# Optimization experiments

Measured on AMD Instinct MI355X. Metric: run time of the kernel, lower is better.

## Reference

```python
import jax, jax.numpy as jnp
import numpy as np

N = 50000        # nodes
E = 400000       # edges (avg degree 8)
T = 4            # edge types
D_IN = 64        # input feature dim
D_OUT = 128      # GGNN hidden / output dim
B = 64           # graphs in batch
STEPS = 8        # GRU propagation steps


def setup_inputs() -> dict:
    key = jax.random.key(0)
    ks = jax.random.split(key, 10)
    s = 1.0 / np.sqrt(D_OUT)
    features = jax.random.normal(ks[0], (N, D_IN), jnp.float32)
    src = jax.random.randint(ks[1], (E,), 0, N, jnp.int32)
    dst = jax.random.randint(ks[2], (E,), 0, N, jnp.int32)
    etype = jax.random.randint(ks[3], (E,), 0, T, jnp.int32)
    node2graph = jnp.sort(jax.random.randint(ks[4], (N,), 0, B, jnp.int32))
    # per-edge-type message Linear(out, out)
    W_msg = jax.random.normal(ks[5], (T, D_OUT, D_OUT), jnp.float32) * s
    b_msg = jnp.zeros((T, D_OUT), jnp.float32)
    # GRUCell(out, out): gate order (r, z, n) as in torch
    w_ih = jax.random.normal(ks[6], (D_OUT, 3 * D_OUT), jnp.float32) * s
    b_ih = jnp.zeros((3 * D_OUT,), jnp.float32)
    w_hh = jax.random.normal(ks[7], (D_OUT, 3 * D_OUT), jnp.float32) * s
    b_hh = jnp.zeros((3 * D_OUT,), jnp.float32)
    # classifier Linear(out, 2)
    W_cls = jax.random.normal(ks[8], (D_OUT, 2), jnp.float32) * s
    b_cls = jnp.zeros((2,), jnp.float32)
    return {"features": features, "src": src, "dst": dst, "etype": etype,
            "node2graph": node2graph, "W_msg": W_msg, "b_msg": b_msg,
            "w_ih": w_ih, "b_ih": b_ih, "w_hh": w_hh, "b_hh": b_hh,
            "W_cls": W_cls, "b_cls": b_cls}


def reference(features, src, dst, etype, node2graph, W_msg, b_msg,
              w_ih, b_ih, w_hh, b_hh, W_cls, b_cls):
    n = features.shape[0]
    # zero-pad input features to D_OUT (as in GGNN.forward)
    h1 = jnp.concatenate(
        [features, jnp.zeros((n, D_OUT - D_IN), features.dtype)], axis=-1)

    def step(h, _):
        # transform every node by every etype weight: [N, T, D]
        t = jnp.einsum('nd,tde->nte', h, W_msg) + b_msg
        msgs = t[src, etype]                       # [E, D] gather per edge
        a = jax.ops.segment_sum(msgs, dst, num_segments=n)  # scatter-sum
        # torch GRUCell(a, h), gates ordered (r, z, n)
        gi = a @ w_ih + b_ih
        gh = h @ w_hh + b_hh
        i_r, i_z, i_n = jnp.split(gi, 3, axis=-1)
        h_r, h_z, h_n = jnp.split(gh, 3, axis=-1)
        r = jax.nn.sigmoid(i_r + h_r)
        z = jax.nn.sigmoid(i_z + h_z)
        ng = jnp.tanh(i_n + r * h_n)
        return (1.0 - z) * ng + z * h, None

    h, _ = jax.lax.scan(step, h1, None, length=STEPS)
    hres = h + h1                                   # residual as in forward
    # read_out == 'sum': per-graph segment sum (dgl.sum_nodes)
    feats_g = jax.ops.segment_sum(hres, node2graph, num_segments=B)  # [B, D]
    return feats_g @ W_cls + b_cls                  # [B, 2]
```

## Files before the change

kernel.cpp:

```cpp
#include <hip/hip_runtime.h>
#include <hip/hip_bf16.h>
#include <math.h>

#define NN 50000
#define EE 400000
#define TT 4
#define DIN 64
#define DD 128
#define BB 64
#define STEPS 8
#define KAGG 544
#define NGATES 512
#define NBIN (4 * NN)
#define NBLK ((NBIN + 255) / 256)
#define MT64 ((NN + 63) / 64)
#define W2F_N (21 * 12288)

typedef __attribute__((ext_vector_type(8))) short bf16x8;
typedef __attribute__((ext_vector_type(4))) float f32x4;
typedef __attribute__((address_space(3))) void lds_void;
typedef __attribute__((address_space(1))) void glob_void;

__device__ inline float bf2f(__hip_bfloat16 x) { return __bfloat162float(x); }

__device__ inline float s2f(short s) {
    unsigned int u = ((unsigned int)(unsigned short)s) << 16;
    float f;
    __builtin_memcpy(&f, &u, 4);
    return f;
}

__global__ void k_init_h(const float* __restrict__ feat, float* __restrict__ h1,
                         __hip_bfloat16* __restrict__ hb) {
    int idx = blockIdx.x * blockDim.x + threadIdx.x;
    if (idx >= NN * DD) return;
    int v = idx >> 7, d = idx & 127;
    float val = (d < DIN) ? feat[v * DIN + d] : 0.0f;
    h1[idx] = val;
    hb[idx] = __float2bfloat16(val);
}

__global__ void k_zero_i32(int* __restrict__ p, int n) {
    int idx = blockIdx.x * blockDim.x + threadIdx.x;
    if (idx < n) p[idx] = 0;
}
__global__ void k_zero_f32(float* __restrict__ p, int n) {
    int idx = blockIdx.x * blockDim.x + threadIdx.x;
    if (idx < n) p[idx] = 0.0f;
}

__global__ void k_hist(const int* __restrict__ dst, const int* __restrict__ etype,
                       int* __restrict__ deg2) {
    int e = blockIdx.x * blockDim.x + threadIdx.x;
    if (e < EE) atomicAdd(&deg2[dst[e] * 4 + etype[e]], 1);
}

__global__ __launch_bounds__(256) void k_scan_bsum(const int* __restrict__ deg2,
                                                   int* __restrict__ bsum) {
    __shared__ int red[256];
    int tid = threadIdx.x;
    int i = blockIdx.x * 256 + tid;
    int v = (i < NBIN) ? deg2[i] : 0;
    red[tid] = v;
    __syncthreads();
#pragma unroll
    for (int s = 128; s > 0; s >>= 1) {
        if (tid < s) red[tid] += red[tid + s];
        __syncthreads();
    }
    if (tid == 0) bsum[blockIdx.x] = red[0];
}

__global__ __launch_bounds__(1024) void k_scan_boff(const int* __restrict__ bsum,
                                                    int* __restrict__ boff) {
    __shared__ int s[1024];
    int tid = threadIdx.x;
    int v = (tid < NBLK) ? bsum[tid] : 0;
    s[tid] = v;
    __syncthreads();
    for (int d = 1; d < 1024; d <<= 1) {
        int t = (tid >= d) ? s[tid - d] : 0;
        __syncthreads();
        s[tid] += t;
        __syncthreads();
    }
    if (tid < NBLK) boff[tid] = s[tid] - v;
}

__global__ __launch_bounds__(256) void k_scan_final(const int* __restrict__ deg2,
                                                    const int* __restrict__ boff,
                                                    int* __restrict__ off2,
                                                    int* __restrict__ cursor) {
    __shared__ int s[256];
    int tid = threadIdx.x;
    int i = blockIdx.x * 256 + tid;
    int v = (i < NBIN) ? deg2[i] : 0;
    s[tid] = v;
    __syncthreads();
#pragma unroll
    for (int d = 1; d < 256; d <<= 1) {
        int t = (tid >= d) ? s[tid - d] : 0;
        __syncthreads();
        s[tid] += t;
        __syncthreads();
    }
    int excl = boff[blockIdx.x] + s[tid] - v;
    if (i < NBIN) {
        off2[i] = excl;
        cursor[i] = excl;
        if (i == NBIN - 1) off2[NBIN] = excl + v;
    }
}

__global__ void k_fill(const int* __restrict__ dst, const int* __restrict__ src,
                       const int* __restrict__ etype, int* __restrict__ cursor,
                       int* __restrict__ csr_src) {
    int e = blockIdx.x * blockDim.x + threadIdx.x;
    if (e < EE) {
        int pos = atomicAdd(&cursor[dst[e] * 4 + etype[e]], 1);
        csr_src[pos] = src[e];
    }
}

__global__ void k_counts(const int* __restrict__ off2, __hip_bfloat16* __restrict__ g) {
    int idx = blockIdx.x * blockDim.x + threadIdx.x;
    if (idx >= NN * 16) return;
    int v = idx >> 4, j = idx & 15;
    float x = 0.0f, y = 0.0f;
    if (j < 2) {
        int t0 = 2 * j;
        x = (float)(off2[4 * v + t0 + 1] - off2[4 * v + t0]);
        y = (float)(off2[4 * v + t0 + 2] - off2[4 * v + t0 + 1]);
    }
    __hip_bfloat162 o;
    o.x = __float2bfloat16(x);
    o.y = __float2bfloat16(y);
    ((__hip_bfloat162*)(g + (size_t)v * KAGG))[256 + j] = o;
}

__global__ void k_prep_w2f(const float* __restrict__ Wm, const float* __restrict__ bm,
                           const float* __restrict__ wih, const float* __restrict__ whh,
                           const float* __restrict__ bih, const float* __restrict__ bhh,
                           __hip_bfloat16* __restrict__ W2f, float* __restrict__ bias512) {
    int idx = blockIdx.x * blockDim.x + threadIdx.x;
    if (idx < W2F_N) {
        int kc = idx / 12288;
        int r1 = idx % 12288;
        int gb = r1 >> 12;
        int r2 = r1 & 4095;
        int w = r2 >> 9;
        int r3 = r2 & 511;
        int l = r3 >> 3;
        int j = r3 & 7;
        int npart = w * 16 + (l & 15);
        int kin = ((l >> 4) << 3) + j;
        float v = 0.0f;
        if (kc < 17) {
            int k = kc * 32 + kin;
            int n = gb * 128 + npart;
            if (k < 512) {
                int t = k >> 7, kd = k & 127;
                const float* wr = Wm + (t << 14) + (kd << 7);
                float s = 0.0f;
#pragma unroll 4
                for (int e = 0; e < 128; ++e) s += wr[e] * wih[e * 384 + n];
                v = s;
            } else if (k < 516) {
                const float* br = bm + ((k - 512) << 7);
                float s = 0.0f;
#pragma unroll 4
                for (int e = 0; e < 128; ++e) s += br[e] * wih[e * 384 + n];
                v = s;
            }
        } else {
            int kh = (kc - 17) * 32 + kin;
            int nlog = (gb < 2) ? gb * 128 + npart : 384 + npart;
            int col = (nlog < 256) ? nlog : nlog - 128;
            v = whh[kh * 384 + col];
        }
        W2f[idx] = __float2bfloat16(v);
        return;
    }
    int b = idx - W2F_N;
    if (b < NGATES) {
        float v;
        if (b < 256) v = bih[b] + bhh[b];
        else if (b < 384) v = bih[b];
        else v = bhh[b - 128];
        bias512[b] = v;
    }
}

__global__ __launch_bounds__(256) void k_agg(const __hip_bfloat16* __restrict__ hb,
                                             const int* __restrict__ off2,
                                             const int* __restrict__ csr_src,
                                             __hip_bfloat16* __restrict__ g) {
    const int node = (blockIdx.x * blockDim.x + threadIdx.x) >> 6;
    const int lane = threadIdx.x & 63;
    if (node >= NN) return;
    const int t = lane >> 4;
    const int sub = lane & 15;
    const int p0 = off2[4 * node + t];
    const int p1 = off2[4 * node + t + 1];
    float a[8];
#pragma unroll
    for (int j = 0; j < 8; ++j) a[j] = 0.0f;
    int p = p0;
    for (; p + 1 < p1; p += 2) {
        int s0 = csr_src[p];
        int s1 = csr_src[p + 1];
        bf16x8 v0 = *(const bf16x8*)(hb + (size_t)s0 * DD + sub * 8);
        bf16x8 v1 = *(const bf16x8*)(hb + (size_t)s1 * DD + sub * 8);
#pragma unroll
        for (int j = 0; j < 8; ++j) a[j] += s2f(v0[j]) + s2f(v1[j]);
    }
    if (p < p1) {
        int s0 = csr_src[p];
        bf16x8 v0 = *(const bf16x8*)(hb + (size_t)s0 * DD + sub * 8);
#pragma unroll
        for (int j = 0; j < 8; ++j) a[j] += s2f(v0[j]);
    }
    bf16x8 o;
#pragma unroll
    for (int j = 0; j < 8; ++j) {
        __hip_bfloat16 b = __float2bfloat16(a[j]);
        o[j] = *(short*)&b;
    }
    *(bf16x8*)(g + (size_t)node * KAGG + t * 128 + sub * 8) = o;
}

__global__ __launch_bounds__(512, 4) void k_step(const __hip_bfloat16* __restrict__ g,
                                                 const __hip_bfloat16* __restrict__ W2f,
                                                 const float* __restrict__ bias512,
                                                 const __hip_bfloat16* __restrict__ hbi,
                                                 __hip_bfloat16* __restrict__ hbo) {
    __shared__ __align__(16) short As[2][64 * 32];
    __shared__ __align__(16) short Ht[64 * 132];
    const int tid = threadIdx.x;
    const int lane = tid & 63;
    const int wave = tid >> 6;
    const int row0 = blockIdx.x * 64;
    const int quad = lane >> 4;
    const int m16 = lane & 15;
    const int koff = ((quad ^ ((m16 ^ (m16 >> 2)) & 3)) << 3);

    const int arow = tid >> 2;
    const int apart = (tid & 3) ^ ((arow ^ (arow >> 2)) & 3);
    int agrow = row0 + arow;
    if (agrow >= NN) agrow = NN - 1;
    const __hip_bfloat16* gA = g + (size_t)agrow * KAGG + apart * 8;
    const __hip_bfloat16* hA = hbi + (size_t)agrow * DD + apart * 8;
    const __hip_bfloat16* bw = W2f + ((size_t)(wave * 64 + lane)) * 8;

    auto stage_A = [&](int kc) {
        if (wave < 4) {
            const glob_void* srcA = (kc < 17)
                                        ? (const glob_void*)(gA + kc * 32)
                                        : (const glob_void*)(hA + (kc - 17) * 32);
            __builtin_amdgcn_global_load_lds(srcA, (lds_void*)&As[kc & 1][(wave * 64) * 8],
                                             16, 0, 0);
        }
    };

    f32x4 acc[4][4];
#pragma unroll
    for (int rt = 0; rt < 4; ++rt)
#pragma unroll
        for (int c = 0; c < 4; ++c) acc[rt][c] = (f32x4){0.f, 0.f, 0.f, 0.f};

    stage_A(0);
    __syncthreads();

    for (int ki = 0; ki < 21; ++ki) {
        if (ki + 1 < 21) stage_A(ki + 1);

        const __hip_bfloat16* bp = bw + ki * 12288;
        bf16x8 b0 = *(const bf16x8*)(bp);
        bf16x8 b1 = *(const bf16x8*)(bp + 4096);
        bf16x8 b2 = *(const bf16x8*)(bp + 8192);

        bf16x8 af[4];
#pragma unroll
        for (int rt = 0; rt < 4; ++rt)
            af[rt] = *(const bf16x8*)&As[ki & 1][(rt * 16 + m16) * 32 + koff];
#pragma unroll
        for (int rt = 0; rt < 4; ++rt)
            acc[rt][0] = __builtin_amdgcn_mfma_f32_16x16x32_bf16(af[rt], b0, acc[rt][0], 0, 0, 0);
#pragma unroll
        for (int rt = 0; rt < 4; ++rt)
            acc[rt][1] = __builtin_amdgcn_mfma_f32_16x16x32_bf16(af[rt], b1, acc[rt][1], 0, 0, 0);
        if (ki < 17) {
#pragma unroll
            for (int rt = 0; rt < 4; ++rt)
                acc[rt][2] = __builtin_amdgcn_mfma_f32_16x16x32_bf16(af[rt], b2, acc[rt][2], 0, 0, 0);
        } else {
#pragma unroll
            for (int rt = 0; rt < 4; ++rt)
                acc[rt][3] = __builtin_amdgcn_mfma_f32_16x16x32_bf16(af[rt], b2, acc[rt][3], 0, 0, 0);
        }
        __syncthreads();
    }

    {
        const int d = wave * 16 + m16;
        const float brs = bias512[d];
        const float bzs = bias512[128 + d];
        const float bin_ = bias512[256 + d];
        const float bhn = bias512[384 + d];
#pragma unroll
        for (int rt = 0; rt < 4; ++rt) {
#pragma unroll
            for (int j = 0; j < 4; ++j) {
                const int rowl = rt * 16 + quad * 4 + j;
                const int grow = row0 + rowl;
                const float rs = acc[rt][0][j] + brs;
                const float zs = acc[rt][1][j] + bzs;
                const float inn = acc[rt][2][j] + bin_;
                const float hnn = acc[rt][3][j] + bhn;
                const float rr = 1.0f / (1.0f + __expf(-rs));
                const float zz = 1.0f / (1.0f + __expf(-zs));
                const float ex = __expf(2.0f * (inn + rr * hnn));
                const float ng = 1.0f - 2.0f / (ex + 1.0f);
                const float hv =
                    bf2f(hbi[(size_t)(grow < NN ? grow : NN - 1) * DD + d]);
                const float o = (1.0f - zz) * ng + zz * hv;
                __hip_bfloat16 ob = __float2bfloat16(o);
                Ht[rowl * 132 + d] = *(short*)&ob;
            }
        }
    }
    __syncthreads();
    {
        const int row = tid >> 3;
        const int col = (tid & 7) * 16;
        if (row0 + row < NN) {
            bf16x8 v0 = *(const bf16x8*)&Ht[row * 132 + col];
            bf16x8 v1 = *(const bf16x8*)&Ht[row * 132 + col + 8];
            __hip_bfloat16* dstp = hbo + (size_t)(row0 + row) * DD + col;
            *(bf16x8*)dstp = v0;
            *(bf16x8*)(dstp + 8) = v1;
        }
    }
}

__global__ __launch_bounds__(128) void k_readout(const __hip_bfloat16* __restrict__ h,
                                                 const float* __restrict__ h1,
                                                 const int* __restrict__ n2g,
                                                 float* __restrict__ feats) {
    const int CHN = 64;
    int d = threadIdx.x;
    int v0 = blockIdx.x * CHN;
    if (v0 >= NN) return;
    int v1 = v0 + CHN;
    if (v1 > NN) v1 = NN;
    float sum = 0.0f;
    int cur = n2g[v0];
    for (int v = v0; v < v1; ++v) {
        int gph = n2g[v];
        if (gph != cur) {
            atomicAdd(&feats[cur * DD + d], sum);
            sum = 0.0f;
            cur = gph;
        }
        sum += bf2f(h[(size_t)v * DD + d]) + h1[(size_t)v * DD + d];
    }
    atomicAdd(&feats[cur * DD + d], sum);
}

__global__ void k_cls(const float* __restrict__ feats, const float* __restrict__ Wc,
                      const float* __restrict__ bc, float* __restrict__ out) {
    int t = threadIdx.x;
    if (t >= BB * 2) return;
    int b = t >> 1, c = t & 1;
    float s = bc[c];
    for (int d = 0; d < DD; ++d) s += feats[b * DD + d] * Wc[d * 2 + c];
    out[t] = s;
}

extern "C" void kernel_launch(void* const* d_in, const int* in_sizes, int n_in, void* d_out,
                              int out_size, void* d_ws, size_t ws_size, hipStream_t stream) {
    const float* features = (const float*)d_in[0];
    const int* src = (const int*)d_in[1];
    const int* dst = (const int*)d_in[2];
    const int* etype = (const int*)d_in[3];
    const int* n2g = (const int*)d_in[4];
    const float* W_msg = (const float*)d_in[5];
    const float* b_msg = (const float*)d_in[6];
    const float* w_ih = (const float*)d_in[7];
    const float* b_ih = (const float*)d_in[8];
    const float* w_hh = (const float*)d_in[9];
    const float* b_hh = (const float*)d_in[10];
    const float* W_cls = (const float*)d_in[11];
    const float* b_cls = (const float*)d_in[12];
    float* out = (float*)d_out;

    char* ws = (char*)d_ws;
    size_t o = 0;
    auto alloc = [&](size_t bytes) {
        o = (o + 255) & ~(size_t)255;
        void* p = ws + o;
        o += bytes;
        return p;
    };
    int* deg2 = (int*)alloc(sizeof(int) * NBIN);
    int* off2 = (int*)alloc(sizeof(int) * (NBIN + 1));
    int* cursor = (int*)alloc(sizeof(int) * NBIN);
    int* bsum = (int*)alloc(sizeof(int) * NBLK);
    int* boff = (int*)alloc(sizeof(int) * NBLK);
    int* csr_src = (int*)alloc(sizeof(int) * EE);
    __hip_bfloat16* W2f = (__hip_bfloat16*)alloc(sizeof(__hip_bfloat16) * W2F_N);
    float* bias512 = (float*)alloc(sizeof(float) * NGATES);
    float* hini = (float*)alloc(sizeof(float) * (size_t)NN * DD);
    __hip_bfloat16* hbfA = (__hip_bfloat16*)alloc(sizeof(__hip_bfloat16) * (size_t)NN * DD);
    __hip_bfloat16* hbfB = (__hip_bfloat16*)alloc(sizeof(__hip_bfloat16) * (size_t)NN * DD);
    __hip_bfloat16* g = (__hip_bfloat16*)alloc(sizeof(__hip_bfloat16) * (size_t)NN * KAGG);
    float* feats = (float*)alloc(sizeof(float) * BB * DD);

    k_init_h<<<(NN * DD + 255) / 256, 256, 0, stream>>>(features, hini, hbfA);
    k_zero_i32<<<(NBIN + 255) / 256, 256, 0, stream>>>(deg2, NBIN);
    k_zero_f32<<<(BB * DD + 255) / 256, 256, 0, stream>>>(feats, BB * DD);
    k_hist<<<(EE + 255) / 256, 256, 0, stream>>>(dst, etype, deg2);
    k_scan_bsum<<<NBLK, 256, 0, stream>>>(deg2, bsum);
    k_scan_boff<<<1, 1024, 0, stream>>>(bsum, boff);
    k_scan_final<<<NBLK, 256, 0, stream>>>(deg2, boff, off2, cursor);
    k_fill<<<(EE + 255) / 256, 256, 0, stream>>>(dst, src, etype, cursor, csr_src);
    k_counts<<<(NN * 16 + 255) / 256, 256, 0, stream>>>(off2, g);
    {
        int prep_n = W2F_N + NGATES;
        k_prep_w2f<<<(prep_n + 255) / 256, 256, 0, stream>>>(W_msg, b_msg, w_ih, w_hh,
                                                             b_ih, b_hh, W2f, bias512);
    }

    __hip_bfloat16* hbc = hbfA;
    __hip_bfloat16* hbx = hbfB;
    for (int s = 0; s < STEPS; ++s) {
        k_agg<<<(NN * 64 + 255) / 256, 256, 0, stream>>>(hbc, off2, csr_src, g);
        k_step<<<MT64, 512, 0, stream>>>(g, W2f, bias512, hbc, hbx);
        __hip_bfloat16* tb = hbc; hbc = hbx; hbx = tb;
    }
    k_readout<<<(NN + 63) / 64, 128, 0, stream>>>(hbc, hini, n2g, feats);
    k_cls<<<1, 128, 0, stream>>>(feats, W_cls, b_cls, out);
}
```

Before: 753.3 us.

## Apply per-type degree bias in GRU epilogue and batch CSR index loads via shuffles

The per-edge-type degree counts are no longer stored as extra K columns of the aggregation matrix. Each count is multiplied by a precomputed bias-times-w_ih matrix in the k_step epilogue, which reads off2 directly. This shrinks the aggregation row from 544 to 512 elements and removes one K-chunk of MFMA work per step, plus the k_counts kernel. Separately, k_agg now loads up to 16 neighbor indices in a single coalesced read and broadcasts them with shuffles instead of issuing a scalar load per edge. The cost is extra global reads of off2 and more FMAs in the epilogue.

```diff
diff --git a/kernel.cpp b/kernel.cpp
--- a/kernel.cpp
+++ b/kernel.cpp
@@ -9,12 +9,12 @@
 #define DD 128
 #define BB 64
 #define STEPS 8
-#define KAGG 544
+#define KAGG 512
 #define NGATES 512
 #define NBIN (4 * NN)
 #define NBLK ((NBIN + 255) / 256)
 #define MT64 ((NN + 63) / 64)
-#define W2F_N (21 * 12288)
+#define W2F_N (20 * 12288)
 
 typedef __attribute__((ext_vector_type(8))) short bf16x8;
 typedef __attribute__((ext_vector_type(4))) float f32x4;
@@ -122,26 +122,11 @@
     }
 }
 
-__global__ void k_counts(const int* __restrict__ off2, __hip_bfloat16* __restrict__ g) {
-    int idx = blockIdx.x * blockDim.x + threadIdx.x;
-    if (idx >= NN * 16) return;
-    int v = idx >> 4, j = idx & 15;
-    float x = 0.0f, y = 0.0f;
-    if (j < 2) {
-        int t0 = 2 * j;
-        x = (float)(off2[4 * v + t0 + 1] - off2[4 * v + t0]);
-        y = (float)(off2[4 * v + t0 + 2] - off2[4 * v + t0 + 1]);
-    }
-    __hip_bfloat162 o;
-    o.x = __float2bfloat16(x);
-    o.y = __float2bfloat16(y);
-    ((__hip_bfloat162*)(g + (size_t)v * KAGG))[256 + j] = o;
-}
-
 __global__ void k_prep_w2f(const float* __restrict__ Wm, const float* __restrict__ bm,
                            const float* __restrict__ wih, const float* __restrict__ whh,
                            const float* __restrict__ bih, const float* __restrict__ bhh,
-                           __hip_bfloat16* __restrict__ W2f, float* __restrict__ bias512) {
+                           __hip_bfloat16* __restrict__ W2f, float* __restrict__ Cmat,
+                           float* __restrict__ bias512) {
     int idx = blockIdx.x * blockDim.x + threadIdx.x;
     if (idx < W2F_N) {
         int kc = idx / 12288;
@@ -154,26 +139,18 @@
         int j = r3 & 7;
         int npart = w * 16 + (l & 15);
         int kin = ((l >> 4) << 3) + j;
-        float v = 0.0f;
-        if (kc < 17) {
+        float v;
+        if (kc < 16) {
             int k = kc * 32 + kin;
             int n = gb * 128 + npart;
-            if (k < 512) {
-                int t = k >> 7, kd = k & 127;
-                const float* wr = Wm + (t << 14) + (kd << 7);
-                float s = 0.0f;
+            int t = k >> 7, kd = k & 127;
+            const float* wr = Wm + (t << 14) + (kd << 7);
+            float s = 0.0f;
 #pragma unroll 4
-                for (int e = 0; e < 128; ++e) s += wr[e] * wih[e * 384 + n];
-                v = s;
-            } else if (k < 516) {
-                const float* br = bm + ((k - 512) << 7);
-                float s = 0.0f;
-#pragma unroll 4
-                for (int e = 0; e < 128; ++e) s += br[e] * wih[e * 384 + n];
-                v = s;
-            }
+            for (int e = 0; e < 128; ++e) s += wr[e] * wih[e * 384 + n];
+            v = s;
         } else {
-            int kh = (kc - 17) * 32 + kin;
+            int kh = (kc - 16) * 32 + kin;
             int nlog = (gb < 2) ? gb * 128 + npart : 384 + npart;
             int col = (nlog < 256) ? nlog : nlog - 128;
             v = whh[kh * 384 + col];
@@ -181,7 +158,17 @@
         W2f[idx] = __float2bfloat16(v);
         return;
     }
-    int b = idx - W2F_N;
+    int j2 = idx - W2F_N;
+    if (j2 < 4 * 384) {
+        int t = j2 / 384, n = j2 % 384;
+        const float* br = bm + t * 128;
+        float s = 0.0f;
+#pragma unroll 4
+        for (int e = 0; e < 128; ++e) s += br[e] * wih[e * 384 + n];
+        Cmat[j2] = s;
+        return;
+    }
+    int b = j2 - 4 * 384;
     if (b < NGATES) {
         float v;
         if (b < 256) v = bih[b] + bhh[b];
@@ -200,25 +187,31 @@
     if (node >= NN) return;
     const int t = lane >> 4;
     const int sub = lane & 15;
+    const int gbase = lane & 48;
     const int p0 = off2[4 * node + t];
     const int p1 = off2[4 * node + t + 1];
     float a[8];
 #pragma unroll
     for (int j = 0; j < 8; ++j) a[j] = 0.0f;
-    int p = p0;
-    for (; p + 1 < p1; p += 2) {
-        int s0 = csr_src[p];
-        int s1 = csr_src[p + 1];
-        bf16x8 v0 = *(const bf16x8*)(hb + (size_t)s0 * DD + sub * 8);
-        bf16x8 v1 = *(const bf16x8*)(hb + (size_t)s1 * DD + sub * 8);
-#pragma unroll
-        for (int j = 0; j < 8; ++j) a[j] += s2f(v0[j]) + s2f(v1[j]);
-    }
-    if (p < p1) {
-        int s0 = csr_src[p];
-        bf16x8 v0 = *(const bf16x8*)(hb + (size_t)s0 * DD + sub * 8);
-#pragma unroll
-        for (int j = 0; j < 8; ++j) a[j] += s2f(v0[j]);
+    for (int base = p0; base < p1; base += 16) {
+        int cnt = p1 - base;
+        if (cnt > 16) cnt = 16;
+        int idxv = (sub < cnt) ? csr_src[base + sub] : 0;
+        int r = 0;
+        for (; r + 1 < cnt; r += 2) {
+            int s0 = __shfl(idxv, gbase + r);
+            int s1 = __shfl(idxv, gbase + r + 1);
+            bf16x8 v0 = *(const bf16x8*)(hb + (size_t)s0 * DD + sub * 8);
+            bf16x8 v1 = *(const bf16x8*)(hb + (size_t)s1 * DD + sub * 8);
+#pragma unroll
+            for (int j = 0; j < 8; ++j) a[j] += s2f(v0[j]) + s2f(v1[j]);
+        }
+        if (r < cnt) {
+            int s0 = __shfl(idxv, gbase + r);
+            bf16x8 v0 = *(const bf16x8*)(hb + (size_t)s0 * DD + sub * 8);
+#pragma unroll
+            for (int j = 0; j < 8; ++j) a[j] += s2f(v0[j]);
+        }
     }
     bf16x8 o;
 #pragma unroll
@@ -231,7 +224,9 @@
 
 __global__ __launch_bounds__(512, 4) void k_step(const __hip_bfloat16* __restrict__ g,
                                                  const __hip_bfloat16* __restrict__ W2f,
+                                                 const float* __restrict__ Cmat,
                                                  const float* __restrict__ bias512,
+                                                 const int* __restrict__ off2,
                                                  const __hip_bfloat16* __restrict__ hbi,
                                                  __hip_bfloat16* __restrict__ hbo) {
     __shared__ __align__(16) short As[2][64 * 32];
@@ -254,9 +249,9 @@
 
     auto stage_A = [&](int kc) {
         if (wave < 4) {
-            const glob_void* srcA = (kc < 17)
+            const glob_void* srcA = (kc < 16)
                                         ? (const glob_void*)(gA + kc * 32)
-                                        : (const glob_void*)(hA + (kc - 17) * 32);
+                                        : (const glob_void*)(hA + (kc - 16) * 32);
             __builtin_amdgcn_global_load_lds(srcA, (lds_void*)&As[kc & 1][(wave * 64) * 8],
                                              16, 0, 0);
         }
@@ -271,8 +266,8 @@
     stage_A(0);
     __syncthreads();
 
-    for (int ki = 0; ki < 21; ++ki) {
-        if (ki + 1 < 21) stage_A(ki + 1);
+    for (int ki = 0; ki < 20; ++ki) {
+        if (ki + 1 < 20) stage_A(ki + 1);
 
         const __hip_bfloat16* bp = bw + ki * 12288;
         bf16x8 b0 = *(const bf16x8*)(bp);
@@ -289,7 +284,7 @@
 #pragma unroll
         for (int rt = 0; rt < 4; ++rt)
             acc[rt][1] = __builtin_amdgcn_mfma_f32_16x16x32_bf16(af[rt], b1, acc[rt][1], 0, 0, 0);
-        if (ki < 17) {
+        if (ki < 16) {
 #pragma unroll
             for (int rt = 0; rt < 4; ++rt)
                 acc[rt][2] = __builtin_amdgcn_mfma_f32_16x16x32_bf16(af[rt], b2, acc[rt][2], 0, 0, 0);
@@ -307,22 +302,30 @@
         const float bzs = bias512[128 + d];
         const float bin_ = bias512[256 + d];
         const float bhn = bias512[384 + d];
+        const float c0r = Cmat[d], c1r = Cmat[384 + d], c2r = Cmat[768 + d], c3r = Cmat[1152 + d];
+        const float c0z = Cmat[128 + d], c1z = Cmat[512 + d], c2z = Cmat[896 + d], c3z = Cmat[1280 + d];
+        const float c0n = Cmat[256 + d], c1n = Cmat[640 + d], c2n = Cmat[1024 + d], c3n = Cmat[1408 + d];
 #pragma unroll
         for (int rt = 0; rt < 4; ++rt) {
 #pragma unroll
             for (int j = 0; j < 4; ++j) {
                 const int rowl = rt * 16 + quad * 4 + j;
-                const int grow = row0 + rowl;
-                const float rs = acc[rt][0][j] + brs;
-                const float zs = acc[rt][1][j] + bzs;
-                const float inn = acc[rt][2][j] + bin_;
+                int grow = row0 + rowl;
+                if (grow >= NN) grow = NN - 1;
+                const int* o2 = off2 + 4 * grow;
+                const float cnt0 = (float)(o2[1] - o2[0]);
+                const float cnt1 = (float)(o2[2] - o2[1]);
+                const float cnt2 = (float)(o2[3] - o2[2]);
+                const float cnt3 = (float)(o2[4] - o2[3]);
+                const float rs = acc[rt][0][j] + brs + cnt0 * c0r + cnt1 * c1r + cnt2 * c2r + cnt3 * c3r;
+                const float zs = acc[rt][1][j] + bzs + cnt0 * c0z + cnt1 * c1z + cnt2 * c2z + cnt3 * c3z;
+                const float inn = acc[rt][2][j] + bin_ + cnt0 * c0n + cnt1 * c1n + cnt2 * c2n + cnt3 * c3n;
                 const float hnn = acc[rt][3][j] + bhn;
                 const float rr = 1.0f / (1.0f + __expf(-rs));
                 const float zz = 1.0f / (1.0f + __expf(-zs));
                 const float ex = __expf(2.0f * (inn + rr * hnn));
                 const float ng = 1.0f - 2.0f / (ex + 1.0f);
-                const float hv =
-                    bf2f(hbi[(size_t)(grow < NN ? grow : NN - 1) * DD + d]);
+                const float hv = bf2f(hbi[(size_t)grow * DD + d]);
                 const float o = (1.0f - zz) * ng + zz * hv;
                 __hip_bfloat16 ob = __float2bfloat16(o);
                 Ht[rowl * 132 + d] = *(short*)&ob;
@@ -409,6 +412,7 @@
     int* boff = (int*)alloc(sizeof(int) * NBLK);
     int* csr_src = (int*)alloc(sizeof(int) * EE);
     __hip_bfloat16* W2f = (__hip_bfloat16*)alloc(sizeof(__hip_bfloat16) * W2F_N);
+    float* Cmat = (float*)alloc(sizeof(float) * 4 * 384);
     float* bias512 = (float*)alloc(sizeof(float) * NGATES);
     float* hini = (float*)alloc(sizeof(float) * (size_t)NN * DD);
     __hip_bfloat16* hbfA = (__hip_bfloat16*)alloc(sizeof(__hip_bfloat16) * (size_t)NN * DD);
@@ -424,18 +428,17 @@
     k_scan_boff<<<1, 1024, 0, stream>>>(bsum, boff);
     k_scan_final<<<NBLK, 256, 0, stream>>>(deg2, boff, off2, cursor);
     k_fill<<<(EE + 255) / 256, 256, 0, stream>>>(dst, src, etype, cursor, csr_src);
-    k_counts<<<(NN * 16 + 255) / 256, 256, 0, stream>>>(off2, g);
     {
-        int prep_n = W2F_N + NGATES;
+        int prep_n = W2F_N + 4 * 384 + NGATES;
         k_prep_w2f<<<(prep_n + 255) / 256, 256, 0, stream>>>(W_msg, b_msg, w_ih, w_hh,
-                                                             b_ih, b_hh, W2f, bias512);
+                                                             b_ih, b_hh, W2f, Cmat, bias512);
     }
 
     __hip_bfloat16* hbc = hbfA;
     __hip_bfloat16* hbx = hbfB;
     for (int s = 0; s < STEPS; ++s) {
         k_agg<<<(NN * 64 + 255) / 256, 256, 0, stream>>>(hbc, off2, csr_src, g);
-        k_step<<<MT64, 512, 0, stream>>>(g, W2f, bias512, hbc, hbx);
+        k_step<<<MT64, 512, 0, stream>>>(g, W2f, Cmat, bias512, off2, hbc, hbx);
         __hip_bfloat16* tb = hbc; hbc = hbx; hbx = tb;
     }
     k_readout<<<(NN + 63) / 64, 128, 0, stream>>>(hbc, hini, n2g, feats);
```

Result: slower. 771.6 us (+2.4%).
